# Kernel optimization log

Hardware: AMD Instinct MI355X
Metric: run time of the kernel (lower is better)

The kernel has to match this reference:

```python
import jax, jax.numpy as jnp
import numpy as np

TOPK = 8
EPS = 1e-12  # matches torch F.normalize default eps


def setup_inputs() -> dict:
    key = jax.random.key(0)
    x = jax.random.normal(key, (8, 2048, 128), dtype=jnp.float32)
    return {"x": x}


def reference(x) -> jnp.ndarray:
    B, N, D = x.shape
    # --- pairwise dot scores on L2-normalized features (cosine similarity) ---
    norm = jnp.sqrt(jnp.sum(x * x, axis=-1, keepdims=True))
    normed = x / jnp.maximum(norm, EPS)
    scores = jnp.einsum('bnd,bmd->bnm', normed, normed)  # [B, N, N]

    # --- top-k per row -> binary adjacency via scatter ---
    _, idx = jax.lax.top_k(scores, TOPK)  # [B, N, k]
    bi = jnp.arange(B)[:, None, None]
    ni = jnp.arange(N)[None, :, None]
    adj = jnp.zeros((B, N, N), dtype=x.dtype).at[bi, ni, idx].set(1.0)

    # --- symmetrize and add self loops ---
    adj = jnp.maximum(adj, jnp.swapaxes(adj, 1, 2))
    eye = jnp.eye(N, dtype=x.dtype)
    adj = jnp.maximum(adj, eye[None, :, :])
    return adj
```

## Files before the change

### kernel.cpp

```cpp
#include <hip/hip_runtime.h>
#include <cstdint>

#define NN 2048
#define DD 128
#define BATCH 8
#define NROWS 16384
#define MARGIN 0.02f
#define CAP 64

typedef __attribute__((ext_vector_type(8))) short bf16x8;
typedef __attribute__((ext_vector_type(4))) float f32x4;
typedef unsigned long long u64;
typedef unsigned int u32;
typedef unsigned short u16;

__device__ __forceinline__ u32 bf16rne(float f) {
  u32 u = __float_as_uint(f);
  return (u + 0x7fffu + ((u >> 16) & 1u)) >> 16;
}

__global__ __launch_bounds__(256) void k_normalize(const float* __restrict__ x,
                                                   double* __restrict__ rinv,
                                                   u32* __restrict__ nb) {
  const int wave = threadIdx.x >> 6, lane = threadIdx.x & 63;
  const long long row = (long long)blockIdx.x * 4 + wave;
  float2 v = ((const float2*)(x + row * DD))[lane];
  const double d0 = v.x, d1 = v.y;
  double s = d0 * d0 + d1 * d1;
  #pragma unroll
  for (int m = 32; m >= 1; m >>= 1) s += __shfl_xor(s, m, 64);
  double den = sqrt(s); den = den > 1e-12 ? den : 1e-12;
  if (lane == 0) rinv[row] = 1.0 / den;
  double2 o; o.x = d0 / den; o.y = d1 / den;
  nb[row * (DD / 2) + lane] = bf16rne((float)o.x) | (bf16rne((float)o.y) << 16);
}

#define CXF(i, j) { const float a_ = L[i], b_ = L[j]; L[i] = fmaxf(a_, b_); L[j] = fminf(a_, b_); }
__device__ __forceinline__ void merge8f(float (&kv)[8], const float (&ov)[8]) {
  float L[8];
  #pragma unroll
  for (int i = 0; i < 8; ++i) L[i] = fmaxf(kv[i], ov[7 - i]);
  CXF(0, 4) CXF(1, 5) CXF(2, 6) CXF(3, 7)
  CXF(0, 2) CXF(1, 3) CXF(4, 6) CXF(5, 7)
  CXF(0, 1) CXF(2, 3) CXF(4, 5) CXF(6, 7)
  #pragma unroll
  for (int i = 0; i < 8; ++i) kv[i] = L[i];
}

__device__ __forceinline__ u64 make_key(double s, int col) {
  u64 u = (u64)__double_as_longlong(s);
  const u64 m = (u64)((long long)u >> 63);
  u ^= (m | 0x8000000000000000ull);
  return (u & ~2047ull) | (u64)(2047 - col);
}
__device__ __forceinline__ u64 umax64(u64 a, u64 b) { return a > b ? a : b; }
__device__ __forceinline__ u64 umin64(u64 a, u64 b) { return a > b ? b : a; }
__device__ __forceinline__ void merge8(u64 (&kv)[8], const u64 (&ov)[8]) {
  u64 L[8];
  #pragma unroll
  for (int i = 0; i < 8; ++i) L[i] = umax64(kv[i], ov[7 - i]);
#define CX(i, j) { const u64 a_ = L[i], b_ = L[j]; L[i] = umax64(a_, b_); L[j] = umin64(a_, b_); }
  CX(0, 4) CX(1, 5) CX(2, 6) CX(3, 7)
  CX(0, 2) CX(1, 3) CX(4, 6) CX(5, 7)
  CX(0, 1) CX(2, 3) CX(4, 5) CX(6, 7)
#undef CX
  #pragma unroll
  for (int i = 0; i < 8; ++i) kv[i] = L[i];
}
__device__ __forceinline__ void insert8u(u64 (&v)[8], u64 nk) {
  if (nk > v[7]) {
    v[7] = nk;
    #pragma unroll
    for (int q = 7; q >= 1; --q) {
      const u64 a = v[q - 1], b = v[q];
      const bool sw = b > a;
      v[q - 1] = sw ? b : a; v[q] = sw ? a : b;
    }
  }
}

__global__ __launch_bounds__(256) void k_gram(const u32* __restrict__ nb,
                                              u16* __restrict__ scores,
                                              u16* __restrict__ bmaxg,
                                              float4* __restrict__ outz) {
  __shared__ u16 bml[4][64][16];
  const int tid = threadIdx.x; const int w = tid >> 6; const int l = tid & 63;
  const int q = l >> 4; const int m = l & 15;
  bf16x8 pvals = {0,0,0,0,0,0,0,0}, pones = {0,0,0,0,0,0,0,0};
  if (q == 0) {
    pvals[0] = (short)(__float_as_uint((float)(m + 1)) >> 16);
    pones[0] = (short)(__float_as_uint(1.0f) >> 16);
  }
  const f32x4 z4 = {0.0f, 0.0f, 0.0f, 0.0f};
  const f32x4 pr  = __builtin_amdgcn_mfma_f32_16x16x32_bf16(pvals, pones, z4, 0, 0, 0);
  const f32x4 pr2 = __builtin_amdgcn_mfma_f32_16x16x32_bf16(pones, pvals, z4, 0, 0, 0);
  int cof[4];
  #pragma unroll
  for (int p = 0; p < 4; ++p) cof[p] = (int)pr[p] - 1;
  const int rof = (int)pr2[0] - 1;
  const bool contig = (cof[1] == cof[0] + 1) && (cof[2] == cof[0] + 2) &&
                      (cof[3] == cof[0] + 3) && ((cof[0] & 3) == 0);
  const int rowblk = blockIdx.x >> 2; const int split = blockIdx.x & 3;
  const int row0 = rowblk * 64;
  const int b = rowblk >> 5;
  const int c0w = split * 512 + w * 128;
  const u32* Bb = nb + ((long long)b * NN + c0w) * (DD / 2);

  bf16x8 ar4[4][4];
  #pragma unroll
  for (int rf = 0; rf < 4; ++rf) {
    const u32* Ap = nb + (long long)(row0 + 16 * rf + m) * (DD / 2) + 4 * q;
    #pragma unroll
    for (int cc = 0; cc < 4; ++cc) ar4[rf][cc] = *(const bf16x8*)(Ap + 16 * cc);
  }
  u16* rowb[4];
  #pragma unroll
  for (int rf = 0; rf < 4; ++rf)
    rowb[rf] = scores + (long long)(row0 + 16 * rf + rof) * NN + c0w;

  bf16x8 bcA[4], bcB[4];

#define LOADB(DST, T) { const u32* p_ = Bb + (long long)(16 * (T) + m) * (DD / 2) + 4 * q; \
  _Pragma("unroll") for (int cc = 0; cc < 4; ++cc) DST[cc] = *(const bf16x8*)(p_ + 16 * cc); }
#define STOREB(ACC, T, RF) { u16* sp = rowb[RF] + 16 * (T);                        \
    if (contig) {                                                                  \
      uint2 sv;                                                                    \
      sv.x = bf16rne(ACC[0]) | (bf16rne(ACC[1]) << 16);                            \
      sv.y = bf16rne(ACC[2]) | (bf16rne(ACC[3]) << 16);                            \
      *(uint2*)(sp + cof[0]) = sv;                                                 \
    } else {                                                                       \
      sp[cof[0]] = (u16)bf16rne(ACC[0]); sp[cof[1]] = (u16)bf16rne(ACC[1]);        \
      sp[cof[2]] = (u16)bf16rne(ACC[2]); sp[cof[3]] = (u16)bf16rne(ACC[3]);        \
    }                                                                              \
    float bm_ = fmaxf(fmaxf(ACC[0], ACC[1]), fmaxf(ACC[2], ACC[3]));               \
    bm_ = fmaxf(bm_, __shfl_xor(bm_, 16, 64));                                     \
    bm_ = fmaxf(bm_, __shfl_xor(bm_, 32, 64));                                     \
    if (q == 0) bml[w][16 * (RF) + m][T] = (u16)bf16rne(bm_); }
#define TILE(BC, T) {                                                              \
    _Pragma("unroll") for (int rf = 0; rf < 4; ++rf) {                             \
      f32x4 acc = z4;                                                              \
      _Pragma("unroll") for (int cc = 0; cc < 4; ++cc)                             \
        acc = __builtin_amdgcn_mfma_f32_16x16x32_bf16(BC[cc], ar4[rf][cc], acc, 0, 0, 0); \
      STOREB(acc, T, rf)                                                           \
    } }

  LOADB(bcA, 0)
  #pragma unroll
  for (int t = 0; t < 8; t += 2) {
    LOADB(bcB, t + 1)
    TILE(bcA, t)
    if (t + 2 < 8) LOADB(bcA, t + 2)
    TILE(bcB, t + 1)
  }
#undef LOADB
#undef STOREB
#undef TILE

  {
    const uint4 v = *(const uint4*)&bml[w][l][0];
    *(uint4*)(bmaxg + ((long long)split * 16384 + row0 + l) * 32 + w * 8) = v;
  }

  {
    const int base = blockIdx.x * 256 + tid;
    const float4 zf = {0.0f, 0.0f, 0.0f, 0.0f};
    #pragma unroll 8
    for (int k = 0; k < 32; ++k) outz[base + k * 262144] = zf;
  }
}

__global__ __launch_bounds__(256) void k_topk_exact(const u16* __restrict__ scores,
                                                    const u16* __restrict__ bmaxg,
                                                    const float* __restrict__ x,
                                                    const double* __restrict__ rinv,
                                                    float* __restrict__ out) {
  __shared__ u32 scnt[4];
  __shared__ u32 sblkn[4];
  __shared__ u32 sblk[4][CAP];
  __shared__ u32 scand[4][CAP];

  const int w = threadIdx.x >> 6, l = threadIdx.x & 63;
  const int r = blockIdx.x * 4 + w;
  const int n = r & (NN - 1);
  const long long brow = r - n;

  if (l == 0) { scnt[w] = 0u; sblkn[w] = 0u; }

  const int s_ = l >> 4, idx_ = l & 15;
  const u32 bm2 = *(const u32*)(bmaxg + ((long long)s_ * 16384 + r) * 32 + 2 * idx_);
  const float b0 = __uint_as_float(bm2 << 16);
  const float b1 = __uint_as_float(bm2 & 0xFFFF0000u);
  const int blk0 = s_ * 32 + 2 * idx_;
  float mx = fmaxf(b0, b1);

  float kv8[8];
  {
    const float o  = __shfl_xor(mx, 1, 64);
    const float h2 = fmaxf(mx, o), l2 = fminf(mx, o);
    const float p0 = __shfl_xor(h2, 2, 64), p1 = __shfl_xor(l2, 2, 64);
    const float m0 = fmaxf(h2, p0);
    const float xx = fminf(h2, p0);
    const float yy = fmaxf(l2, p1);
    const float m3 = fminf(l2, p1);
    const float m1 = fmaxf(xx, yy);
    const float m2 = fminf(xx, yy);
    const float q0 = __shfl_xor(m0, 4, 64), q1 = __shfl_xor(m1, 4, 64);
    const float q2 = __shfl_xor(m2, 4, 64), q3 = __shfl_xor(m3, 4, 64);
    float L[8] = {m0, m1, m2, m3, q3, q2, q1, q0};
    CXF(0, 4) CXF(1, 5) CXF(2, 6) CXF(3, 7)
    CXF(0, 2) CXF(1, 3) CXF(4, 6) CXF(5, 7)
    CXF(0, 1) CXF(2, 3) CXF(4, 5) CXF(6, 7)
    #pragma unroll
    for (int s = 0; s < 8; ++s) kv8[s] = L[s];
    #pragma unroll
    for (int mk = 8; mk <= 32; mk <<= 1) {
      float ov[8];
      #pragma unroll
      for (int s = 0; s < 8; ++s) ov[s] = __shfl_xor(kv8[s], mk, 64);
      merge8f(kv8, ov);
    }
  }
  const float th = kv8[7] - MARGIN;

  if (b0 >= th) { const u32 id = atomicAdd(&sblkn[w], 1u); if (id < CAP) sblk[w][id] = (u32)blk0; }
  if (b1 >= th) { const u32 id = atomicAdd(&sblkn[w], 1u); if (id < CAP) sblk[w][id] = (u32)(blk0 + 1); }

  int c;
  const int nbq = (int)sblkn[w];
  const u16* rowp = scores + (long long)r * NN;
  if (nbq <= CAP) {
    for (int i = 0; i < nbq; i += 4) {
      const int bi = i + s_;
      const u32 blk = (bi < nbq) ? sblk[w][bi] : sblk[w][0];
      const int col = (int)blk * 16 + idx_;
      const float v = __uint_as_float((u32)rowp[col] << 16);
      if (bi < nbq && v >= th) {
        const u32 id = atomicAdd(&scnt[w], 1u);
        if (id < CAP) scand[w][id] = (u32)col;
      }
    }
    c = (int)scnt[w];
  } else {
    c = CAP + 1;
  }

  const double ri = rinv[r];
  u64 kv[8];
  #pragma unroll
  for (int s = 0; s < 8; ++s) kv[s] = 0ull;

  if (c <= CAP) {
    float2 a4[4];
    #pragma unroll
    for (int j = 0; j < 4; ++j)
      a4[j] = ((const float2*)(x + (long long)r * DD))[idx_ + 16 * j];

    for (int i = 0; i < c; i += 4) {
      const int gi = i + s_;
      const bool valid = gi < c;
      const int col = valid ? ((int)scand[w][gi] & (NN - 1)) : 0;
      const float2* cp = (const float2*)(x + (brow + col) * DD);
      double d = 0.0;
      #pragma unroll
      for (int j = 0; j < 4; ++j) {
        const float2 bv = cp[idx_ + 16 * j];
        d = fma((double)a4[j].x, (double)bv.x, d);
        d = fma((double)a4[j].y, (double)bv.y, d);
      }
      #pragma unroll
      for (int mk = 1; mk <= 8; mk <<= 1) d += __shfl_xor(d, mk, 64);
      if (valid) insert8u(kv, make_key(d * ri * rinv[brow + col], col));
    }
    #pragma unroll
    for (int mk = 16; mk <= 32; mk <<= 1) {
      u64 ov[8];
      #pragma unroll
      for (int s = 0; s < 8; ++s) ov[s] = __shfl_xor(kv[s], mk, 64);
      merge8(kv, ov);
    }
  } else {
    for (int base = 0; base < NN; base += 64) {
      const int col = base + l;
      const float* ap = x + (long long)r * DD;
      const float* cp = x + (brow + col) * DD;
      double d = 0.0;
      for (int kk = 0; kk < 64; ++kk) {
        const float2 av = ((const float2*)ap)[kk];
        const float2 bv = ((const float2*)cp)[kk];
        d = fma((double)av.x, (double)bv.x, fma((double)av.y, (double)bv.y, d));
      }
      d = d * ri * rinv[brow + col];
      u64 one[8];
      one[0] = make_key(d, col);
      #pragma unroll
      for (int s = 1; s < 8; ++s) one[s] = 0ull;
      #pragma unroll
      for (int mk = 1; mk <= 32; mk <<= 1) {
        u64 ov[8];
        #pragma unroll
        for (int s = 0; s < 8; ++s) ov[s] = __shfl_xor(one[s], mk, 64);
        merge8(one, ov);
      }
      merge8(kv, one);
    }
  }

  const long long orow = (long long)r * NN;
  const long long obase = brow * NN;
  if (l == 8) out[orow + n] = 1.0f;
  #pragma unroll
  for (int s = 0; s < 8; ++s) {
    const int mcol = 2047 - (int)(kv[s] & 2047ull);
    if (l == s) {
      out[orow + mcol] = 1.0f;
      out[obase + (long long)mcol * NN + n] = 1.0f;
    }
  }
}

extern "C" void kernel_launch(void* const* d_in, const int* in_sizes, int n_in,
                              void* d_out, int out_size, void* d_ws, size_t ws_size,
                              hipStream_t stream) {
  const float* x = (const float*)d_in[0];
  float* out = (float*)d_out;
  char* ws = (char*)d_ws;
  u32* nb = (u32*)ws;
  double* rinv = (double*)(ws + 4194304);
  u16* scores = (u16*)(ws + 4325376);
  u16* bmaxg = (u16*)(ws + 71434240);

  hipLaunchKernelGGL(k_normalize, dim3(NROWS / 4), dim3(256), 0, stream, x, rinv, nb);
  hipLaunchKernelGGL(k_gram, dim3(1024), dim3(256), 0, stream, nb, scores, bmaxg,
                     (float4*)out);
  hipLaunchKernelGGL(k_topk_exact, dim3(NROWS / 4), dim3(256), 0, stream, scores, bmaxg, x, rinv, out);
}
```

Baseline: 248.1 us.

## Drop bf16 score matrix; recompute Gram in top-k kernel with threshold filtering

The gram kernel now writes only per-block maxima and no longer stores the full bf16 score matrix to workspace. The top-k kernel recomputes the Gram tile with MFMA per 64-row block, using thresholds derived from the block maxima, and collects candidates directly into shared memory. This removes a large score-matrix write and read at the cost of computing the bf16 Gram twice. The top-k grid shrinks to 256 blocks of 512 threads, which may limit occupancy. Candidate capacity drops to 48 and falls back to the full exact scan on overflow.

```diff
diff --git a/kernel.cpp b/kernel.cpp
--- a/kernel.cpp
+++ b/kernel.cpp
@@ -6,7 +6,7 @@
 #define BATCH 8
 #define NROWS 16384
 #define MARGIN 0.02f
-#define CAP 64
+#define CAP2 48
 
 typedef __attribute__((ext_vector_type(8))) short bf16x8;
 typedef __attribute__((ext_vector_type(4))) float f32x4;
@@ -79,27 +79,13 @@
   }
 }
 
-__global__ __launch_bounds__(256) void k_gram(const u32* __restrict__ nb,
-                                              u16* __restrict__ scores,
-                                              u16* __restrict__ bmaxg,
-                                              float4* __restrict__ outz) {
+__global__ __launch_bounds__(256) void k_gram_bmax(const u32* __restrict__ nb,
+                                                   u16* __restrict__ bmaxg,
+                                                   float4* __restrict__ outz) {
   __shared__ u16 bml[4][64][16];
   const int tid = threadIdx.x; const int w = tid >> 6; const int l = tid & 63;
   const int q = l >> 4; const int m = l & 15;
-  bf16x8 pvals = {0,0,0,0,0,0,0,0}, pones = {0,0,0,0,0,0,0,0};
-  if (q == 0) {
-    pvals[0] = (short)(__float_as_uint((float)(m + 1)) >> 16);
-    pones[0] = (short)(__float_as_uint(1.0f) >> 16);
-  }
   const f32x4 z4 = {0.0f, 0.0f, 0.0f, 0.0f};
-  const f32x4 pr  = __builtin_amdgcn_mfma_f32_16x16x32_bf16(pvals, pones, z4, 0, 0, 0);
-  const f32x4 pr2 = __builtin_amdgcn_mfma_f32_16x16x32_bf16(pones, pvals, z4, 0, 0, 0);
-  int cof[4];
-  #pragma unroll
-  for (int p = 0; p < 4; ++p) cof[p] = (int)pr[p] - 1;
-  const int rof = (int)pr2[0] - 1;
-  const bool contig = (cof[1] == cof[0] + 1) && (cof[2] == cof[0] + 2) &&
-                      (cof[3] == cof[0] + 3) && ((cof[0] & 3) == 0);
   const int rowblk = blockIdx.x >> 2; const int split = blockIdx.x & 3;
   const int row0 = rowblk * 64;
   const int b = rowblk >> 5;
@@ -113,48 +99,31 @@
     #pragma unroll
     for (int cc = 0; cc < 4; ++cc) ar4[rf][cc] = *(const bf16x8*)(Ap + 16 * cc);
   }
-  u16* rowb[4];
-  #pragma unroll
-  for (int rf = 0; rf < 4; ++rf)
-    rowb[rf] = scores + (long long)(row0 + 16 * rf + rof) * NN + c0w;
-
   bf16x8 bcA[4], bcB[4];
 
 #define LOADB(DST, T) { const u32* p_ = Bb + (long long)(16 * (T) + m) * (DD / 2) + 4 * q; \
   _Pragma("unroll") for (int cc = 0; cc < 4; ++cc) DST[cc] = *(const bf16x8*)(p_ + 16 * cc); }
-#define STOREB(ACC, T, RF) { u16* sp = rowb[RF] + 16 * (T);                        \
-    if (contig) {                                                                  \
-      uint2 sv;                                                                    \
-      sv.x = bf16rne(ACC[0]) | (bf16rne(ACC[1]) << 16);                            \
-      sv.y = bf16rne(ACC[2]) | (bf16rne(ACC[3]) << 16);                            \
-      *(uint2*)(sp + cof[0]) = sv;                                                 \
-    } else {                                                                       \
-      sp[cof[0]] = (u16)bf16rne(ACC[0]); sp[cof[1]] = (u16)bf16rne(ACC[1]);        \
-      sp[cof[2]] = (u16)bf16rne(ACC[2]); sp[cof[3]] = (u16)bf16rne(ACC[3]);        \
-    }                                                                              \
-    float bm_ = fmaxf(fmaxf(ACC[0], ACC[1]), fmaxf(ACC[2], ACC[3]));               \
-    bm_ = fmaxf(bm_, __shfl_xor(bm_, 16, 64));                                     \
-    bm_ = fmaxf(bm_, __shfl_xor(bm_, 32, 64));                                     \
-    if (q == 0) bml[w][16 * (RF) + m][T] = (u16)bf16rne(bm_); }
-#define TILE(BC, T) {                                                              \
+#define TILE1(BC, T) {                                                             \
     _Pragma("unroll") for (int rf = 0; rf < 4; ++rf) {                             \
       f32x4 acc = z4;                                                              \
       _Pragma("unroll") for (int cc = 0; cc < 4; ++cc)                             \
         acc = __builtin_amdgcn_mfma_f32_16x16x32_bf16(BC[cc], ar4[rf][cc], acc, 0, 0, 0); \
-      STOREB(acc, T, rf)                                                           \
+      float bm_ = fmaxf(fmaxf(acc[0], acc[1]), fmaxf(acc[2], acc[3]));             \
+      bm_ = fmaxf(bm_, __shfl_xor(bm_, 16, 64));                                   \
+      bm_ = fmaxf(bm_, __shfl_xor(bm_, 32, 64));                                   \
+      if (q == 0) bml[w][16 * rf + m][T] = (u16)bf16rne(bm_);                      \
     } }
 
   LOADB(bcA, 0)
   #pragma unroll
   for (int t = 0; t < 8; t += 2) {
     LOADB(bcB, t + 1)
-    TILE(bcA, t)
+    TILE1(bcA, t)
     if (t + 2 < 8) LOADB(bcA, t + 2)
-    TILE(bcB, t + 1)
+    TILE1(bcB, t + 1)
   }
 #undef LOADB
-#undef STOREB
-#undef TILE
+#undef TILE1
 
   {
     const uint4 v = *(const uint4*)&bml[w][l][0];
@@ -169,151 +138,197 @@
   }
 }
 
-__global__ __launch_bounds__(256) void k_topk_exact(const u16* __restrict__ scores,
+__global__ __launch_bounds__(512) void k_topk_fused(const u32* __restrict__ nb,
                                                     const u16* __restrict__ bmaxg,
                                                     const float* __restrict__ x,
                                                     const double* __restrict__ rinv,
                                                     float* __restrict__ out) {
-  __shared__ u32 scnt[4];
-  __shared__ u32 sblkn[4];
-  __shared__ u32 sblk[4][CAP];
-  __shared__ u32 scand[4][CAP];
-
-  const int w = threadIdx.x >> 6, l = threadIdx.x & 63;
-  const int r = blockIdx.x * 4 + w;
-  const int n = r & (NN - 1);
-  const long long brow = r - n;
-
-  if (l == 0) { scnt[w] = 0u; sblkn[w] = 0u; }
-
-  const int s_ = l >> 4, idx_ = l & 15;
-  const u32 bm2 = *(const u32*)(bmaxg + ((long long)s_ * 16384 + r) * 32 + 2 * idx_);
-  const float b0 = __uint_as_float(bm2 << 16);
-  const float b1 = __uint_as_float(bm2 & 0xFFFF0000u);
-  const int blk0 = s_ * 32 + 2 * idx_;
-  float mx = fmaxf(b0, b1);
-
-  float kv8[8];
-  {
-    const float o  = __shfl_xor(mx, 1, 64);
-    const float h2 = fmaxf(mx, o), l2 = fminf(mx, o);
-    const float p0 = __shfl_xor(h2, 2, 64), p1 = __shfl_xor(l2, 2, 64);
-    const float m0 = fmaxf(h2, p0);
-    const float xx = fminf(h2, p0);
-    const float yy = fmaxf(l2, p1);
-    const float m3 = fminf(l2, p1);
-    const float m1 = fmaxf(xx, yy);
-    const float m2 = fminf(xx, yy);
-    const float q0 = __shfl_xor(m0, 4, 64), q1 = __shfl_xor(m1, 4, 64);
-    const float q2 = __shfl_xor(m2, 4, 64), q3 = __shfl_xor(m3, 4, 64);
-    float L[8] = {m0, m1, m2, m3, q3, q2, q1, q0};
-    CXF(0, 4) CXF(1, 5) CXF(2, 6) CXF(3, 7)
-    CXF(0, 2) CXF(1, 3) CXF(4, 6) CXF(5, 7)
-    CXF(0, 1) CXF(2, 3) CXF(4, 5) CXF(6, 7)
-    #pragma unroll
-    for (int s = 0; s < 8; ++s) kv8[s] = L[s];
-    #pragma unroll
-    for (int mk = 8; mk <= 32; mk <<= 1) {
-      float ov[8];
+  __shared__ float thl[64];
+  __shared__ u32 cnt[64];
+  __shared__ u32 cand[64][CAP2];
+
+  const int tid = threadIdx.x; const int w = tid >> 6; const int l = tid & 63;
+  const int q = l >> 4; const int m = l & 15;
+  const int s_ = q, idx_ = m;
+  const int rowblk = blockIdx.x;
+  const int row0 = rowblk * 64;
+  const int b = rowblk >> 5;
+  const long long brow = (long long)b * NN;
+
+  bf16x8 pvals = {0,0,0,0,0,0,0,0}, pones = {0,0,0,0,0,0,0,0};
+  if (q == 0) {
+    pvals[0] = (short)(__float_as_uint((float)(m + 1)) >> 16);
+    pones[0] = (short)(__float_as_uint(1.0f) >> 16);
+  }
+  const f32x4 z4 = {0.0f, 0.0f, 0.0f, 0.0f};
+  const f32x4 pr  = __builtin_amdgcn_mfma_f32_16x16x32_bf16(pvals, pones, z4, 0, 0, 0);
+  const f32x4 pr2 = __builtin_amdgcn_mfma_f32_16x16x32_bf16(pones, pvals, z4, 0, 0, 0);
+  int cof[4];
+  #pragma unroll
+  for (int p = 0; p < 4; ++p) cof[p] = (int)pr[p] - 1;
+  const int rof = (int)pr2[0] - 1;
+
+  if (tid < 64) cnt[tid] = 0u;
+
+  for (int j = 0; j < 8; ++j) {
+    const int rib = w * 8 + j;
+    const int row = row0 + rib;
+    const u32 bm2 = *(const u32*)(bmaxg + ((long long)s_ * 16384 + row) * 32 + 2 * idx_);
+    const float b0 = __uint_as_float(bm2 << 16);
+    const float b1 = __uint_as_float(bm2 & 0xFFFF0000u);
+    float mx = fmaxf(b0, b1);
+    float kv8[8];
+    {
+      const float o  = __shfl_xor(mx, 1, 64);
+      const float h2 = fmaxf(mx, o), l2 = fminf(mx, o);
+      const float p0 = __shfl_xor(h2, 2, 64), p1 = __shfl_xor(l2, 2, 64);
+      const float m0 = fmaxf(h2, p0);
+      const float xx = fminf(h2, p0);
+      const float yy = fmaxf(l2, p1);
+      const float m3 = fminf(l2, p1);
+      const float m1 = fmaxf(xx, yy);
+      const float m2 = fminf(xx, yy);
+      const float q0 = __shfl_xor(m0, 4, 64), q1 = __shfl_xor(m1, 4, 64);
+      const float q2 = __shfl_xor(m2, 4, 64), q3 = __shfl_xor(m3, 4, 64);
+      float L[8] = {m0, m1, m2, m3, q3, q2, q1, q0};
+      CXF(0, 4) CXF(1, 5) CXF(2, 6) CXF(3, 7)
+      CXF(0, 2) CXF(1, 3) CXF(4, 6) CXF(5, 7)
+      CXF(0, 1) CXF(2, 3) CXF(4, 5) CXF(6, 7)
       #pragma unroll
-      for (int s = 0; s < 8; ++s) ov[s] = __shfl_xor(kv8[s], mk, 64);
-      merge8f(kv8, ov);
+      for (int s = 0; s < 8; ++s) kv8[s] = L[s];
+      #pragma unroll
+      for (int mk = 8; mk <= 32; mk <<= 1) {
+        float ov[8];
+        #pragma unroll
+        for (int s = 0; s < 8; ++s) ov[s] = __shfl_xor(kv8[s], mk, 64);
+        merge8f(kv8, ov);
+      }
     }
-  }
-  const float th = kv8[7] - MARGIN;
-
-  if (b0 >= th) { const u32 id = atomicAdd(&sblkn[w], 1u); if (id < CAP) sblk[w][id] = (u32)blk0; }
-  if (b1 >= th) { const u32 id = atomicAdd(&sblkn[w], 1u); if (id < CAP) sblk[w][id] = (u32)(blk0 + 1); }
-
-  int c;
-  const int nbq = (int)sblkn[w];
-  const u16* rowp = scores + (long long)r * NN;
-  if (nbq <= CAP) {
-    for (int i = 0; i < nbq; i += 4) {
-      const int bi = i + s_;
-      const u32 blk = (bi < nbq) ? sblk[w][bi] : sblk[w][0];
-      const int col = (int)blk * 16 + idx_;
-      const float v = __uint_as_float((u32)rowp[col] << 16);
-      if (bi < nbq && v >= th) {
-        const u32 id = atomicAdd(&scnt[w], 1u);
-        if (id < CAP) scand[w][id] = (u32)col;
+    if (l == 0) thl[rib] = kv8[7] - MARGIN;
+  }
+  __syncthreads();
+
+  float th4[4]; int rib4[4];
+  #pragma unroll
+  for (int rf = 0; rf < 4; ++rf) {
+    rib4[rf] = 16 * rf + rof;
+    th4[rf] = thl[rib4[rf]];
+  }
+
+  const int c0w = w * 256;
+  const u32* Bb = nb + (brow + c0w) * (DD / 2);
+  bf16x8 ar4[4][4];
+  #pragma unroll
+  for (int rf = 0; rf < 4; ++rf) {
+    const u32* Ap = nb + (long long)(row0 + 16 * rf + m) * (DD / 2) + 4 * q;
+    #pragma unroll
+    for (int cc = 0; cc < 4; ++cc) ar4[rf][cc] = *(const bf16x8*)(Ap + 16 * cc);
+  }
+  bf16x8 bcA[4], bcB[4];
+
+#define LOADB2(DST, T) { const u32* p_ = Bb + (long long)(16 * (T) + m) * (DD / 2) + 4 * q; \
+  _Pragma("unroll") for (int cc = 0; cc < 4; ++cc) DST[cc] = *(const bf16x8*)(p_ + 16 * cc); }
+#define TILEF(BC, T) {                                                             \
+    _Pragma("unroll") for (int rf = 0; rf < 4; ++rf) {                             \
+      f32x4 acc = z4;                                                              \
+      _Pragma("unroll") for (int cc = 0; cc < 4; ++cc)                             \
+        acc = __builtin_amdgcn_mfma_f32_16x16x32_bf16(BC[cc], ar4[rf][cc], acc, 0, 0, 0); \
+      _Pragma("unroll") for (int p = 0; p < 4; ++p) {                              \
+        if (acc[p] >= th4[rf]) {                                                   \
+          const u32 id = atomicAdd(&cnt[rib4[rf]], 1u);                            \
+          if (id < CAP2) cand[rib4[rf]][id] = (u32)(c0w + 16 * (T) + cof[p]);      \
+        }                                                                          \
+      }                                                                            \
+    } }
+
+  LOADB2(bcA, 0)
+  #pragma unroll
+  for (int t = 0; t < 16; t += 2) {
+    LOADB2(bcB, t + 1)
+    TILEF(bcA, t)
+    if (t + 2 < 16) LOADB2(bcA, t + 2)
+    TILEF(bcB, t + 1)
+  }
+#undef LOADB2
+#undef TILEF
+  __syncthreads();
+
+  for (int j = 0; j < 8; ++j) {
+    const int rib = w * 8 + j;
+    const int r = row0 + rib;
+    const int n = r & (NN - 1);
+    const int c = (int)cnt[rib];
+    const double ri = rinv[r];
+    u64 kv[8];
+    #pragma unroll
+    for (int s = 0; s < 8; ++s) kv[s] = 0ull;
+
+    if (c <= CAP2) {
+      float2 a4[4];
+      #pragma unroll
+      for (int jj = 0; jj < 4; ++jj)
+        a4[jj] = ((const float2*)(x + (long long)r * DD))[idx_ + 16 * jj];
+
+      for (int i = 0; i < c; i += 4) {
+        const int gi = i + s_;
+        const bool valid = gi < c;
+        const int col = valid ? (int)cand[rib][gi] : 0;
+        const float2* cp = (const float2*)(x + (brow + col) * DD);
+        double d = 0.0;
+        #pragma unroll
+        for (int jj = 0; jj < 4; ++jj) {
+          const float2 bv = cp[idx_ + 16 * jj];
+          d = fma((double)a4[jj].x, (double)bv.x, d);
+          d = fma((double)a4[jj].y, (double)bv.y, d);
+        }
+        #pragma unroll
+        for (int mk = 1; mk <= 8; mk <<= 1) d += __shfl_xor(d, mk, 64);
+        if (valid) insert8u(kv, make_key(d * ri * rinv[brow + col], col));
+      }
+      #pragma unroll
+      for (int mk = 16; mk <= 32; mk <<= 1) {
+        u64 ov[8];
+        #pragma unroll
+        for (int s = 0; s < 8; ++s) ov[s] = __shfl_xor(kv[s], mk, 64);
+        merge8(kv, ov);
+      }
+    } else {
+      for (int base = 0; base < NN; base += 64) {
+        const int col = base + l;
+        const float* ap = x + (long long)r * DD;
+        const float* cp2 = x + (brow + col) * DD;
+        double d = 0.0;
+        for (int kk = 0; kk < 64; ++kk) {
+          const float2 av = ((const float2*)ap)[kk];
+          const float2 bv = ((const float2*)cp2)[kk];
+          d = fma((double)av.x, (double)bv.x, fma((double)av.y, (double)bv.y, d));
+        }
+        d = d * ri * rinv[brow + col];
+        u64 one[8];
+        one[0] = make_key(d, col);
+        #pragma unroll
+        for (int s = 1; s < 8; ++s) one[s] = 0ull;
+        #pragma unroll
+        for (int mk = 1; mk <= 32; mk <<= 1) {
+          u64 ov[8];
+          #pragma unroll
+          for (int s = 0; s < 8; ++s) ov[s] = __shfl_xor(one[s], mk, 64);
+          merge8(one, ov);
+        }
+        merge8(kv, one);
       }
     }
-    c = (int)scnt[w];
-  } else {
-    c = CAP + 1;
-  }
-
-  const double ri = rinv[r];
-  u64 kv[8];
-  #pragma unroll
-  for (int s = 0; s < 8; ++s) kv[s] = 0ull;
-
-  if (c <= CAP) {
-    float2 a4[4];
-    #pragma unroll
-    for (int j = 0; j < 4; ++j)
-      a4[j] = ((const float2*)(x + (long long)r * DD))[idx_ + 16 * j];
-
-    for (int i = 0; i < c; i += 4) {
-      const int gi = i + s_;
-      const bool valid = gi < c;
-      const int col = valid ? ((int)scand[w][gi] & (NN - 1)) : 0;
-      const float2* cp = (const float2*)(x + (brow + col) * DD);
-      double d = 0.0;
-      #pragma unroll
-      for (int j = 0; j < 4; ++j) {
-        const float2 bv = cp[idx_ + 16 * j];
-        d = fma((double)a4[j].x, (double)bv.x, d);
-        d = fma((double)a4[j].y, (double)bv.y, d);
-      }
-      #pragma unroll
-      for (int mk = 1; mk <= 8; mk <<= 1) d += __shfl_xor(d, mk, 64);
-      if (valid) insert8u(kv, make_key(d * ri * rinv[brow + col], col));
-    }
-    #pragma unroll
-    for (int mk = 16; mk <= 32; mk <<= 1) {
-      u64 ov[8];
-      #pragma unroll
-      for (int s = 0; s < 8; ++s) ov[s] = __shfl_xor(kv[s], mk, 64);
-      merge8(kv, ov);
-    }
-  } else {
-    for (int base = 0; base < NN; base += 64) {
-      const int col = base + l;
-      const float* ap = x + (long long)r * DD;
-      const float* cp = x + (brow + col) * DD;
-      double d = 0.0;
-      for (int kk = 0; kk < 64; ++kk) {
-        const float2 av = ((const float2*)ap)[kk];
-        const float2 bv = ((const float2*)cp)[kk];
-        d = fma((double)av.x, (double)bv.x, fma((double)av.y, (double)bv.y, d));
-      }
-      d = d * ri * rinv[brow + col];
-      u64 one[8];
-      one[0] = make_key(d, col);
-      #pragma unroll
-      for (int s = 1; s < 8; ++s) one[s] = 0ull;
-      #pragma unroll
-      for (int mk = 1; mk <= 32; mk <<= 1) {
-        u64 ov[8];
-        #pragma unroll
-        for (int s = 0; s < 8; ++s) ov[s] = __shfl_xor(one[s], mk, 64);
-        merge8(one, ov);
-      }
-      merge8(kv, one);
-    }
-  }
-
-  const long long orow = (long long)r * NN;
-  const long long obase = brow * NN;
-  if (l == 8) out[orow + n] = 1.0f;
-  #pragma unroll
-  for (int s = 0; s < 8; ++s) {
-    const int mcol = 2047 - (int)(kv[s] & 2047ull);
-    if (l == s) {
-      out[orow + mcol] = 1.0f;
-      out[obase + (long long)mcol * NN + n] = 1.0f;
+
+    const long long orow = (long long)r * NN;
+    const long long obase = brow * NN;
+    if (l == 8) out[orow + n] = 1.0f;
+    #pragma unroll
+    for (int s = 0; s < 8; ++s) {
+      const int mcol = 2047 - (int)(kv[s] & 2047ull);
+      if (l == s) {
+        out[orow + mcol] = 1.0f;
+        out[obase + (long long)mcol * NN + n] = 1.0f;
+      }
     }
   }
 }
@@ -326,11 +341,10 @@
   char* ws = (char*)d_ws;
   u32* nb = (u32*)ws;
   double* rinv = (double*)(ws + 4194304);
-  u16* scores = (u16*)(ws + 4325376);
-  u16* bmaxg = (u16*)(ws + 71434240);
+  u16* bmaxg = (u16*)(ws + 4325376);
 
   hipLaunchKernelGGL(k_normalize, dim3(NROWS / 4), dim3(256), 0, stream, x, rinv, nb);
-  hipLaunchKernelGGL(k_gram, dim3(1024), dim3(256), 0, stream, nb, scores, bmaxg,
+  hipLaunchKernelGGL(k_gram_bmax, dim3(1024), dim3(256), 0, stream, nb, bmaxg,
                      (float4*)out);
-  hipLaunchKernelGGL(k_topk_exact, dim3(NROWS / 4), dim3(256), 0, stream, scores, bmaxg, x, rinv, out);
-}
+  hipLaunchKernelGGL(k_topk_fused, dim3(256), dim3(512), 0, stream, nb, bmaxg, x, rinv, out);
+}
```

Result: no change. 243.7 us (-1.8%).
